# Kernel optimization log

Measured on AMD Instinct MI355X. Metric: run time of the kernel, lower is better.

Reference implementation:

```python
import jax, jax.numpy as jnp
import numpy as np

N_NODES = 50000
N_EDGES = 1600000


def _seg_softmax(e, seg, n):
    # numerically-stable softmax over edges grouped by destination node
    m = jax.ops.segment_max(e, seg, num_segments=n)
    ex = jnp.exp(e - m[seg])
    s = jax.ops.segment_sum(ex, seg, num_segments=n)
    return ex / s[seg]


def setup_inputs() -> dict:
    key = jax.random.key(0)
    ks = jax.random.split(key, 16)
    IN, OUT, ED = 64, 32, 8
    inp = {
        'x': jax.random.normal(ks[0], (N_NODES, IN), jnp.float32),
        'ex': jax.random.normal(ks[1], (N_EDGES, ED), jnp.float32),
        'src': jax.random.randint(ks[2], (N_EDGES,), 0, N_NODES),
        'dst': jax.random.randint(ks[3], (N_EDGES,), 0, N_NODES),
        'W_fc': jax.random.normal(ks[4], (OUT, IN), jnp.float32) * 0.1,
        'b_fc': jax.random.normal(ks[5], (OUT,), jnp.float32) * 0.1,
        'W_att': jax.random.normal(ks[6], (1, 2 * OUT + ED), jnp.float32) * 0.1,
        'b_att': jax.random.normal(ks[7], (1,), jnp.float32) * 0.1,
        'W_edge': jax.random.normal(ks[8], (OUT, ED), jnp.float32) * 0.1,
        'b_edge': jax.random.normal(ks[9], (OUT,), jnp.float32) * 0.1,
        'W_eatt': jax.random.normal(ks[10], (ED, ED), jnp.float32) * 0.1,
        'b_eatt': jax.random.normal(ks[11], (ED,), jnp.float32) * 0.1,
        'W_q': jax.random.normal(ks[12], (OUT, OUT), jnp.float32) * 0.1,
        'b_q': jax.random.normal(ks[13], (OUT,), jnp.float32) * 0.1,
        'W_s': jax.random.normal(ks[14], (OUT, OUT), jnp.float32) * 0.1,
        'b_s': jax.random.normal(ks[15], (OUT,), jnp.float32) * 0.1,
    }
    return inp


def reference(x, ex, src, dst, W_fc, b_fc, W_att, b_att, W_edge, b_edge,
              W_eatt, b_eatt, W_q, b_q, W_s, b_s):
    n = x.shape[0]
    # node transform (fc; batch norm disabled in config)
    z = x @ W_fc.T + b_fc                      # [N, OUT]
    z_src = z[src]                             # [E, OUT]
    z_dst = z[dst]                             # [E, OUT]
    # edge transform for attention score
    ex_t = ex @ W_eatt.T + b_eatt              # [E, ED]
    # edge-dependent attention logit + leaky_relu(0.2)
    z2 = jnp.concatenate([z_src, z_dst, ex_t], axis=1)  # [E, 2*OUT+ED]
    a = z2 @ W_att.T + b_att                   # [E, 1]
    e = jnp.where(a >= 0, a, 0.2 * a)
    # edge feature aggregation transform
    ez = ex @ W_edge.T + b_edge                # [E, OUT]
    # similar_node branch: pointwise conv1d == linear; per-edge dot product
    q = z_src @ W_q.T + b_q                    # query(src)
    s = z_dst @ W_s.T + b_s                    # support(dst)
    es = jnp.sum(q * s, axis=1, keepdims=True)  # [E, 1]
    # edge-softmax over incoming edges of each destination node
    alpha = _seg_softmax(e, dst, n)            # [E, 1]
    similar = _seg_softmax(es, dst, n)         # [E, 1]
    h_att = jax.ops.segment_sum(alpha * z_src, dst, num_segments=n)    # [N, OUT]
    h2 = jax.ops.segment_sum(similar * z_src, dst, num_segments=n)     # [N, OUT]
    h = h_att * h2
    # attention-weighted edge feature aggregation
    h = h + jax.ops.segment_sum(alpha * ez, dst, num_segments=n)
    return h, alpha
```

## Files before the change

kernel.cpp:

```cpp
#include <hip/hip_runtime.h>
#include <hip/hip_fp16.h>

#define OUTF 32
#define INF 64
#define EDF 8
#define CAP 64
#define BSH 7
#define NBKMAX 512
#define EPB 4096

__global__ __launch_bounds__(256) void prep_kernel(
    const float* __restrict__ x,
    const float* __restrict__ W_fc, const float* __restrict__ b_fc,
    const float* __restrict__ W_q,  const float* __restrict__ b_q,
    const float* __restrict__ W_s,  const float* __restrict__ b_s,
    const float* __restrict__ W_att,
    __half* __restrict__ z16, float* __restrict__ t,
    float* __restrict__ c_es,
    float* __restrict__ att_s, float* __restrict__ att_d,
    int* __restrict__ cursor, int* __restrict__ bhist, int n_nodes)
{
    int i = blockIdx.x * 256 + threadIdx.x;
    if (i < NBKMAX) bhist[i] = 0;
    if (i >= n_nodes) return;
    cursor[i] = i * CAP;
    int n = i;

    float xl[INF];
    for (int k = 0; k < INF; k++) xl[k] = x[(size_t)n * INF + k];

    float zl[OUTF];
    float a1 = 0.f, a2 = 0.f;
    for (int o = 0; o < OUTF; o++) {
        float acc = b_fc[o];
        for (int k = 0; k < INF; k++) acc += xl[k] * W_fc[o * INF + k];
        zl[o] = acc;
        z16[(size_t)n * OUTF + o] = __float2half(acc);
        a1 += acc * W_att[o];
        a2 += acc * W_att[OUTF + o];
    }
    att_s[n] = a1;
    att_d[n] = a2;

    float sl[OUTF];
    float ces = 0.f;
    for (int o = 0; o < OUTF; o++) {
        float as = b_s[o];
        for (int k = 0; k < OUTF; k++) as += zl[k] * W_s[o * OUTF + k];
        sl[o] = as;
        ces += b_q[o] * as;
    }
    c_es[n] = ces;
    for (int k = 0; k < OUTF; k++) {
        float tv = 0.f;
        for (int o = 0; o < OUTF; o++) tv += W_q[o * OUTF + k] * sl[o];
        t[(size_t)n * OUTF + k] = tv;
    }
}

__global__ __launch_bounds__(256) void bhist_kernel(
    const int* __restrict__ didx, int* __restrict__ bhist, int eBase, int eEnd)
{
    __shared__ int cnt[NBKMAX];
    for (int i = threadIdx.x; i < NBKMAX; i += 256) cnt[i] = 0;
    __syncthreads();
    int e0 = eBase + blockIdx.x * EPB;
    #pragma unroll 16
    for (int k = 0; k < 16; k++) {
        int e = e0 + k * 256 + threadIdx.x;
        if (e < eEnd) atomicAdd(&cnt[didx[e] >> BSH], 1);
    }
    __syncthreads();
    for (int i = threadIdx.x; i < NBKMAX; i += 256)
        if (cnt[i]) atomicAdd(&bhist[i], cnt[i]);
}

__global__ __launch_bounds__(512) void bscan_kernel(
    int* __restrict__ bhist, int* __restrict__ bbase,
    int* __restrict__ bcursor, int nbk)
{
    __shared__ int sh[512];
    int t = threadIdx.x;
    int v = (t < nbk) ? bhist[t] : 0;
    sh[t] = v;
    __syncthreads();
    for (int st = 1; st < 512; st <<= 1) {
        int tv = (t >= st) ? sh[t - st] : 0;
        __syncthreads();
        sh[t] += tv;
        __syncthreads();
    }
    if (t < nbk) {
        int excl = sh[t] - v;
        bbase[t] = excl;
        bcursor[t] = excl;
        bhist[t] = 0;
        if (t == nbk - 1) bbase[nbk] = sh[t];
    }
}

__global__ __launch_bounds__(256) void bin_kernel(
    const int* __restrict__ sidx, const int* __restrict__ didx,
    int* __restrict__ bcursor, int2* __restrict__ stage, int eBase, int eEnd)
{
    __shared__ int cnt[NBKMAX];
    __shared__ int gbase[NBKMAX];
    for (int i = threadIdx.x; i < NBKMAX; i += 256) cnt[i] = 0;
    __syncthreads();
    int e0 = eBase + blockIdx.x * EPB;
    int srcv[16], dstv[16], rankv[16];
    #pragma unroll 16
    for (int k = 0; k < 16; k++) {
        int e = e0 + k * 256 + threadIdx.x;
        if (e < eEnd) {
            srcv[k] = sidx[e]; dstv[k] = didx[e];
            rankv[k] = atomicAdd(&cnt[dstv[k] >> BSH], 1);
        } else srcv[k] = -1;
    }
    __syncthreads();
    for (int b = threadIdx.x; b < NBKMAX; b += 256)
        if (cnt[b]) gbase[b] = atomicAdd(&bcursor[b], cnt[b]);
    __syncthreads();
    #pragma unroll 16
    for (int k = 0; k < 16; k++) {
        if (srcv[k] >= 0) {
            int e = e0 + k * 256 + threadIdx.x;
            int b = dstv[k] >> BSH;
            stage[gbase[b] + rankv[k]] =
                make_int2(srcv[k], e | ((dstv[k] & 127) << 21));
        }
    }
}

__global__ __launch_bounds__(256) void place_kernel(
    const int* __restrict__ bbase, const int2* __restrict__ stage,
    int2* __restrict__ csr, int* __restrict__ cursor, int N)
{
    __shared__ int c[1 << BSH];
    int b = blockIdx.x;
    int nodeBase = b << BSH;
    int nNodes = min(1 << BSH, N - nodeBase);
    for (int i = threadIdx.x; i < nNodes; i += 256) c[i] = cursor[nodeBase + i];
    __syncthreads();
    int beg = bbase[b], end = bbase[b + 1];
    for (int j = beg + threadIdx.x; j < end; j += 256) {
        int2 r = stage[j];
        int dl  = (r.y >> 21) & 127;
        int eid = r.y & 0x1FFFFF;
        int pos = atomicAdd(&c[dl], 1);
        if (pos < (nodeBase + dl) * CAP + CAP)
            csr[pos] = make_int2(r.x, eid);
    }
    __syncthreads();
    for (int i = threadIdx.x; i < nNodes; i += 256) {
        int lim = (nodeBase + i) * CAP + CAP;
        cursor[nodeBase + i] = min(c[i], lim);
    }
}

__device__ __forceinline__ float4 loadHalf4(const __half* p) {
    uint2 raw = *(const uint2*)p;
    __half2 h01 = *reinterpret_cast<__half2*>(&raw.x);
    __half2 h23 = *reinterpret_cast<__half2*>(&raw.y);
    float2 f01 = __half22float2(h01);
    float2 f23 = __half22float2(h23);
    return make_float4(f01.x, f01.y, f23.x, f23.y);
}

__global__ __launch_bounds__(256) void agg_kernel(
    const int* __restrict__ cursor, const int2* __restrict__ csr,
    const float* __restrict__ att_d, const float* __restrict__ c_es,
    const __half* __restrict__ z16, const float* __restrict__ t,
    const float* __restrict__ ex,
    const float* __restrict__ W_att, const float* __restrict__ b_att,
    const float* __restrict__ W_eatt, const float* __restrict__ b_eatt,
    const float* __restrict__ W_edge, const float* __restrict__ b_edge,
    float* __restrict__ h_out, float* __restrict__ invS_out, int N)
{
    __shared__ float sv3[EDF];
    __shared__ float ccs;
    __shared__ float sWedge[OUTF * EDF];
    __shared__ float sbedge[OUTF];
    int tid = threadIdx.x;
    if (tid < EDF) {
        float a = 0.f;
        for (int j = 0; j < EDF; j++) a += W_att[2 * OUTF + j] * W_eatt[j * EDF + tid];
        sv3[tid] = a;
    }
    if (tid == 0) {
        float a = b_att[0];
        for (int j = 0; j < EDF; j++) a += W_att[2 * OUTF + j] * b_eatt[j];
        ccs = a;
    }
    if (tid < OUTF * EDF) sWedge[tid] = W_edge[tid];
    if (tid < OUTF) sbedge[tid] = b_edge[tid];
    __syncthreads();

    int wave = blockIdx.x * 4 + (tid >> 6);
    if (wave >= N) return;
    int lane = tid & 63;
    int g = lane >> 3;
    int l = lane & 7;
    int n = wave;
    int beg = n * CAP, end = cursor[n];

    float4 t4  = *(const float4*)(t + (size_t)n * OUTF + l * 4);
    float4 wa4 = *(const float4*)(W_att + l * 4);
    float4 v34 = (l < 2) ? *(const float4*)(sv3 + l * 4)
                         : make_float4(0.f, 0.f, 0.f, 0.f);
    float attc = att_d[n] + ccs;
    float cesn = c_es[n];

    float S = 0.f, Spe = 0.f;
    float4 U1 = make_float4(0.f, 0.f, 0.f, 0.f);
    float4 U2 = U1, Uax = U1;

    for (int p0 = beg; p0 < end; p0 += 16) {
        int posA = p0 + g;
        bool vA = posA < end;
        int2 ceA = csr[vA ? posA : beg];
        int posB = p0 + 8 + g;
        bool vB = posB < end;
        int2 ceB = csr[vB ? posB : beg];

        float4 zA = loadHalf4(z16 + (size_t)ceA.x * OUTF + l * 4);
        float4 zB = loadHalf4(z16 + (size_t)ceB.x * OUTF + l * 4);
        float4 eA = (l < 2) ? *(const float4*)(ex + (size_t)ceA.y * EDF + l * 4)
                            : make_float4(0.f, 0.f, 0.f, 0.f);
        float4 eB = (l < 2) ? *(const float4*)(ex + (size_t)ceB.y * EDF + l * 4)
                            : make_float4(0.f, 0.f, 0.f, 0.f);

        float rA = zA.x * t4.x + zA.y * t4.y + zA.z * t4.z + zA.w * t4.w;
        float mA = zA.x * wa4.x + zA.y * wa4.y + zA.z * wa4.z + zA.w * wa4.w
                 + eA.x * v34.x + eA.y * v34.y + eA.z * v34.z + eA.w * v34.w;
        float rB = zB.x * t4.x + zB.y * t4.y + zB.z * t4.z + zB.w * t4.w;
        float mB = zB.x * wa4.x + zB.y * wa4.y + zB.z * wa4.z + zB.w * wa4.w
                 + eB.x * v34.x + eB.y * v34.y + eB.z * v34.z + eB.w * v34.w;
        #pragma unroll
        for (int m = 4; m >= 1; m >>= 1) {
            rA += __shfl_xor(rA, m);
            mA += __shfl_xor(mA, m);
            rB += __shfl_xor(rB, m);
            mB += __shfl_xor(mB, m);
        }
        float aA = mA + attc;
        float aB = mB + attc;
        float pA  = vA ? __expf(aA >= 0.f ? aA : 0.2f * aA) : 0.f;
        float peA = vA ? __expf(rA + cesn) : 0.f;
        float pB  = vB ? __expf(aB >= 0.f ? aB : 0.2f * aB) : 0.f;
        float peB = vB ? __expf(rB + cesn) : 0.f;

        S += pA + pB; Spe += peA + peB;
        U1.x += pA * zA.x + pB * zB.x;  U1.y += pA * zA.y + pB * zB.y;
        U1.z += pA * zA.z + pB * zB.z;  U1.w += pA * zA.w + pB * zB.w;
        U2.x += peA * zA.x + peB * zB.x; U2.y += peA * zA.y + peB * zB.y;
        U2.z += peA * zA.z + peB * zB.z; U2.w += peA * zA.w + peB * zB.w;
        Uax.x += pA * eA.x + pB * eB.x; Uax.y += pA * eA.y + pB * eB.y;
        Uax.z += pA * eA.z + pB * eB.z; Uax.w += pA * eA.w + pB * eB.w;
    }

    #pragma unroll
    for (int m = 8; m <= 32; m <<= 1) {
        S   += __shfl_xor(S, m);
        Spe += __shfl_xor(Spe, m);
        U1.x += __shfl_xor(U1.x, m); U1.y += __shfl_xor(U1.y, m);
        U1.z += __shfl_xor(U1.z, m); U1.w += __shfl_xor(U1.w, m);
        U2.x += __shfl_xor(U2.x, m); U2.y += __shfl_xor(U2.y, m);
        U2.z += __shfl_xor(U2.z, m); U2.w += __shfl_xor(U2.w, m);
        Uax.x += __shfl_xor(Uax.x, m); Uax.y += __shfl_xor(Uax.y, m);
        Uax.z += __shfl_xor(Uax.z, m); Uax.w += __shfl_xor(Uax.w, m);
    }

    float invS = 0.f;
    float4 h4 = make_float4(0.f, 0.f, 0.f, 0.f);
    if (end > beg) {
        invS = 1.f / S;
        float invSpe = 1.f / Spe;
        float ax[EDF];
        ax[0] = __shfl(Uax.x, 0); ax[1] = __shfl(Uax.y, 0);
        ax[2] = __shfl(Uax.z, 0); ax[3] = __shfl(Uax.w, 0);
        ax[4] = __shfl(Uax.x, 1); ax[5] = __shfl(Uax.y, 1);
        ax[6] = __shfl(Uax.z, 1); ax[7] = __shfl(Uax.w, 1);
        #pragma unroll
        for (int j = 0; j < 4; j++) {
            int c = l * 4 + j;
            float hagg = sbedge[c];
            #pragma unroll
            for (int k = 0; k < EDF; k++)
                hagg += sWedge[c * EDF + k] * (ax[k] * invS);
            float hatt = ((j == 0) ? U1.x : (j == 1) ? U1.y : (j == 2) ? U1.z : U1.w) * invS;
            float h2   = ((j == 0) ? U2.x : (j == 1) ? U2.y : (j == 2) ? U2.z : U2.w) * invSpe;
            ((float*)&h4)[j] = hatt * h2 + hagg;
        }
    }
    if (lane < 8) {
        *(float4*)(h_out + (size_t)n * OUTF + l * 4) = h4;
        if (lane == 0) invS_out[n] = invS;
    }
}

__global__ __launch_bounds__(256) void alpha_kernel(
    const int* __restrict__ sidx, const int* __restrict__ didx,
    const float* __restrict__ ex,
    const float* __restrict__ att_s, const float* __restrict__ att_d,
    const float* __restrict__ invS,
    const float* __restrict__ W_att, const float* __restrict__ b_att,
    const float* __restrict__ W_eatt, const float* __restrict__ b_eatt,
    float* __restrict__ alpha_out, int E)
{
    __shared__ float v3[EDF];
    __shared__ float ccs;
    int tid = threadIdx.x;
    if (tid < EDF) {
        float a = 0.f;
        for (int j = 0; j < EDF; j++) a += W_att[2 * OUTF + j] * W_eatt[j * EDF + tid];
        v3[tid] = a;
    }
    if (tid == 0) {
        float a = b_att[0];
        for (int j = 0; j < EDF; j++) a += W_att[2 * OUTF + j] * b_eatt[j];
        ccs = a;
    }
    __syncthreads();

    int e = blockIdx.x * 256 + tid;
    if (e >= E) return;
    int si = sidx[e], di = didx[e];
    const float4* exr = (const float4*)(ex + (size_t)e * EDF);
    float4 e0 = exr[0], e1 = exr[1];
    float a = att_s[si] + att_d[di] + ccs
            + e0.x * v3[0] + e0.y * v3[1] + e0.z * v3[2] + e0.w * v3[3]
            + e1.x * v3[4] + e1.y * v3[5] + e1.z * v3[6] + e1.w * v3[7];
    float el = (a >= 0.f) ? a : 0.2f * a;
    alpha_out[e] = __expf(el) * invS[di];
}

extern "C" void kernel_launch(void* const* d_in, const int* in_sizes, int n_in,
                              void* d_out, int out_size, void* d_ws, size_t ws_size,
                              hipStream_t stream) {
    const float* x      = (const float*)d_in[0];
    const float* ex     = (const float*)d_in[1];
    const int*   sidx   = (const int*)d_in[2];
    const int*   didx   = (const int*)d_in[3];
    const float* W_fc   = (const float*)d_in[4];
    const float* b_fc   = (const float*)d_in[5];
    const float* W_att  = (const float*)d_in[6];
    const float* b_att  = (const float*)d_in[7];
    const float* W_edge = (const float*)d_in[8];
    const float* b_edge = (const float*)d_in[9];
    const float* W_eatt = (const float*)d_in[10];
    const float* b_eatt = (const float*)d_in[11];
    const float* W_q    = (const float*)d_in[12];
    const float* b_q    = (const float*)d_in[13];
    const float* W_s    = (const float*)d_in[14];
    const float* b_s    = (const float*)d_in[15];

    int N = in_sizes[0] / INF;
    int E = in_sizes[2];
    int N32 = N * OUTF;
    int nbk = (N + (1 << BSH) - 1) >> BSH;

    float* h_out     = (float*)d_out;
    float* alpha_out = h_out + N32;

    float*  base    = (float*)d_ws;
    int*    cursor  = (int*)base;
    float*  att_s   = base + N;
    float*  att_d   = att_s + N;
    float*  invS    = att_d + N;
    float*  c_es    = invS + N;
    __half* z16     = (__half*)(c_es + N);
    float*  t       = (float*)(z16 + (size_t)N * OUTF);

    size_t fixedBytes = (size_t)N * (20 + 64 + 128 + CAP * 8) + 8192;
    int halfE = (E + 1) / 2;
    int stageElems = (ws_size >= fixedBytes + (size_t)E * 8) ? E : halfE;
    int phases = (stageElems == E) ? 1 : 2;

    int2*  stage   = (int2*)(t + N32);
    int2*  csr     = stage + stageElems;
    int*   bhist   = (int*)(csr + (size_t)N * CAP);
    int*   bbase   = bhist + NBKMAX;
    int*   bcursor = bbase + NBKMAX + 1;

    prep_kernel<<<(N + 255) / 256, 256, 0, stream>>>(
        x, W_fc, b_fc, W_q, b_q, W_s, b_s, W_att,
        z16, t, c_es, att_s, att_d, cursor, bhist, N);

    for (int ph = 0; ph < phases; ph++) {
        int eB = ph * stageElems;
        int eE = (eB + stageElems < E) ? eB + stageElems : E;
        int nbC = (eE - eB + EPB - 1) / EPB;
        bhist_kernel<<<nbC, 256, 0, stream>>>(didx, bhist, eB, eE);
        bscan_kernel<<<1, 512, 0, stream>>>(bhist, bbase, bcursor, nbk);
        bin_kernel<<<nbC, 256, 0, stream>>>(sidx, didx, bcursor, stage, eB, eE);
        place_kernel<<<nbk, 256, 0, stream>>>(bbase, stage, csr, cursor, N);
    }

    int nbAgg = (N + 3) / 4;
    agg_kernel<<<nbAgg, 256, 0, stream>>>(
        cursor, csr, att_d, c_es,
        z16, t, ex,
        W_att, b_att, W_eatt, b_eatt, W_edge, b_edge,
        h_out, invS, N);

    int nbE = (E + 255) / 256;
    alpha_kernel<<<nbE, 256, 0, stream>>>(
        sidx, didx, ex, att_s, att_d, invS,
        W_att, b_att, W_eatt, b_eatt, alpha_out, E);
}
```

Baseline: 188.1 us.

## Replace fixed-capacity CSR with compact per-node CSR and fp16 staged edge features

Drops the fixed CAP=64 slots per node and instead computes exact per-node offsets with a per-bucket count and scan in place_kernel, producing a compact index list. Edge features are gathered during binning and stored as fp16 in bucket order, so the aggregation reads them from nearly contiguous staging memory instead of doing random fp32 reads of ex. Bucket size is halved to 64 nodes and the two-phase workspace fallback is removed. The risks are that the workspace must now hold all staged data at once, fp16 edge features lose precision, and packing src into 16 bits only works for node ids below 65536.

```diff
diff --git a/kernel.cpp b/kernel.cpp
--- a/kernel.cpp
+++ b/kernel.cpp
@@ -4,9 +4,9 @@
 #define OUTF 32
 #define INF 64
 #define EDF 8
-#define CAP 64
-#define BSH 7
-#define NBKMAX 512
+#define BSH 6
+#define BN  (1 << BSH)
+#define NBKMAX 1024
 #define EPB 4096
 
 __global__ __launch_bounds__(256) void prep_kernel(
@@ -18,12 +18,11 @@
     __half* __restrict__ z16, float* __restrict__ t,
     float* __restrict__ c_es,
     float* __restrict__ att_s, float* __restrict__ att_d,
-    int* __restrict__ cursor, int* __restrict__ bhist, int n_nodes)
+    int* __restrict__ bhist, int n_nodes)
 {
     int i = blockIdx.x * 256 + threadIdx.x;
     if (i < NBKMAX) bhist[i] = 0;
     if (i >= n_nodes) return;
-    cursor[i] = i * CAP;
     int n = i;
 
     float xl[INF];
@@ -59,32 +58,32 @@
 }
 
 __global__ __launch_bounds__(256) void bhist_kernel(
-    const int* __restrict__ didx, int* __restrict__ bhist, int eBase, int eEnd)
+    const int* __restrict__ didx, int* __restrict__ bhist, int E)
 {
     __shared__ int cnt[NBKMAX];
     for (int i = threadIdx.x; i < NBKMAX; i += 256) cnt[i] = 0;
     __syncthreads();
-    int e0 = eBase + blockIdx.x * EPB;
+    int e0 = blockIdx.x * EPB;
     #pragma unroll 16
     for (int k = 0; k < 16; k++) {
         int e = e0 + k * 256 + threadIdx.x;
-        if (e < eEnd) atomicAdd(&cnt[didx[e] >> BSH], 1);
+        if (e < E) atomicAdd(&cnt[didx[e] >> BSH], 1);
     }
     __syncthreads();
     for (int i = threadIdx.x; i < NBKMAX; i += 256)
         if (cnt[i]) atomicAdd(&bhist[i], cnt[i]);
 }
 
-__global__ __launch_bounds__(512) void bscan_kernel(
-    int* __restrict__ bhist, int* __restrict__ bbase,
+__global__ __launch_bounds__(1024) void bscan_kernel(
+    const int* __restrict__ bhist, int* __restrict__ bbase,
     int* __restrict__ bcursor, int nbk)
 {
-    __shared__ int sh[512];
+    __shared__ int sh[1024];
     int t = threadIdx.x;
     int v = (t < nbk) ? bhist[t] : 0;
     sh[t] = v;
     __syncthreads();
-    for (int st = 1; st < 512; st <<= 1) {
+    for (int st = 1; st < 1024; st <<= 1) {
         int tv = (t >= st) ? sh[t - st] : 0;
         __syncthreads();
         sh[t] += tv;
@@ -94,25 +93,31 @@
         int excl = sh[t] - v;
         bbase[t] = excl;
         bcursor[t] = excl;
-        bhist[t] = 0;
         if (t == nbk - 1) bbase[nbk] = sh[t];
     }
+}
+
+__device__ __forceinline__ unsigned pack2h(float a, float b) {
+    __half2 h = __floats2half2_rn(a, b);
+    return *(unsigned*)&h;
 }
 
 __global__ __launch_bounds__(256) void bin_kernel(
     const int* __restrict__ sidx, const int* __restrict__ didx,
-    int* __restrict__ bcursor, int2* __restrict__ stage, int eBase, int eEnd)
+    const float* __restrict__ ex,
+    int* __restrict__ bcursor, int* __restrict__ stage_meta,
+    uint4* __restrict__ stage_ex, int E)
 {
     __shared__ int cnt[NBKMAX];
     __shared__ int gbase[NBKMAX];
     for (int i = threadIdx.x; i < NBKMAX; i += 256) cnt[i] = 0;
     __syncthreads();
-    int e0 = eBase + blockIdx.x * EPB;
+    int e0 = blockIdx.x * EPB;
     int srcv[16], dstv[16], rankv[16];
     #pragma unroll 16
     for (int k = 0; k < 16; k++) {
         int e = e0 + k * 256 + threadIdx.x;
-        if (e < eEnd) {
+        if (e < E) {
             srcv[k] = sidx[e]; dstv[k] = didx[e];
             rankv[k] = atomicAdd(&cnt[dstv[k] >> BSH], 1);
         } else srcv[k] = -1;
@@ -126,35 +131,57 @@
         if (srcv[k] >= 0) {
             int e = e0 + k * 256 + threadIdx.x;
             int b = dstv[k] >> BSH;
-            stage[gbase[b] + rankv[k]] =
-                make_int2(srcv[k], e | ((dstv[k] & 127) << 21));
+            int pos = gbase[b] + rankv[k];
+            stage_meta[pos] = srcv[k] | ((dstv[k] & (BN - 1)) << 16);
+            const float4* exr = (const float4*)(ex + (size_t)e * EDF);
+            float4 a = exr[0], c = exr[1];
+            stage_ex[pos] = make_uint4(pack2h(a.x, a.y), pack2h(a.z, a.w),
+                                       pack2h(c.x, c.y), pack2h(c.z, c.w));
         }
     }
 }
 
 __global__ __launch_bounds__(256) void place_kernel(
-    const int* __restrict__ bbase, const int2* __restrict__ stage,
-    int2* __restrict__ csr, int* __restrict__ cursor, int N)
-{
-    __shared__ int c[1 << BSH];
+    const int* __restrict__ bbase, const int* __restrict__ stage_meta,
+    int* __restrict__ csr_pos, int* __restrict__ nodeStart,
+    int* __restrict__ nodeCnt, int N)
+{
+    __shared__ int cnt[BN], excl[BN], cur[BN], scan[BN];
+    int tid = threadIdx.x;
     int b = blockIdx.x;
     int nodeBase = b << BSH;
-    int nNodes = min(1 << BSH, N - nodeBase);
-    for (int i = threadIdx.x; i < nNodes; i += 256) c[i] = cursor[nodeBase + i];
-    __syncthreads();
     int beg = bbase[b], end = bbase[b + 1];
-    for (int j = beg + threadIdx.x; j < end; j += 256) {
-        int2 r = stage[j];
-        int dl  = (r.y >> 21) & 127;
-        int eid = r.y & 0x1FFFFF;
-        int pos = atomicAdd(&c[dl], 1);
-        if (pos < (nodeBase + dl) * CAP + CAP)
-            csr[pos] = make_int2(r.x, eid);
-    }
-    __syncthreads();
-    for (int i = threadIdx.x; i < nNodes; i += 256) {
-        int lim = (nodeBase + i) * CAP + CAP;
-        cursor[nodeBase + i] = min(c[i], lim);
+
+    if (tid < BN) cnt[tid] = 0;
+    __syncthreads();
+    for (int j = beg + tid; j < end; j += 256)
+        atomicAdd(&cnt[(stage_meta[j] >> 16) & (BN - 1)], 1);
+    __syncthreads();
+    if (tid < BN) scan[tid] = cnt[tid];
+    __syncthreads();
+    for (int st = 1; st < BN; st <<= 1) {
+        int v = (tid < BN && tid >= st) ? scan[tid - st] : 0;
+        __syncthreads();
+        if (tid < BN) scan[tid] += v;
+        __syncthreads();
+    }
+    if (tid < BN) {
+        excl[tid] = scan[tid] - cnt[tid];
+        cur[tid] = excl[tid];
+    }
+    __syncthreads();
+    for (int j = beg + tid; j < end; j += 256) {
+        int dl = (stage_meta[j] >> 16) & (BN - 1);
+        int pos = atomicAdd(&cur[dl], 1);
+        csr_pos[beg + pos] = j;
+    }
+    __syncthreads();
+    if (tid < BN) {
+        int n = nodeBase + tid;
+        if (n < N) {
+            nodeStart[n] = beg + excl[tid];
+            nodeCnt[n] = cnt[tid];
+        }
     }
 }
 
@@ -166,12 +193,17 @@
     float2 f23 = __half22float2(h23);
     return make_float4(f01.x, f01.y, f23.x, f23.y);
 }
+__device__ __forceinline__ float2 unp2(unsigned u) {
+    __half2 h = *reinterpret_cast<__half2*>(&u);
+    return __half22float2(h);
+}
 
 __global__ __launch_bounds__(256) void agg_kernel(
-    const int* __restrict__ cursor, const int2* __restrict__ csr,
+    const int* __restrict__ nodeStart, const int* __restrict__ nodeCnt,
+    const int* __restrict__ csr_pos,
+    const int* __restrict__ stage_meta, const uint4* __restrict__ stage_ex,
     const float* __restrict__ att_d, const float* __restrict__ c_es,
     const __half* __restrict__ z16, const float* __restrict__ t,
-    const float* __restrict__ ex,
     const float* __restrict__ W_att, const float* __restrict__ b_att,
     const float* __restrict__ W_eatt, const float* __restrict__ b_eatt,
     const float* __restrict__ W_edge, const float* __restrict__ b_edge,
@@ -202,7 +234,7 @@
     int g = lane >> 3;
     int l = lane & 7;
     int n = wave;
-    int beg = n * CAP, end = cursor[n];
+    int beg = nodeStart[n], ec = nodeCnt[n];
 
     float4 t4  = *(const float4*)(t + (size_t)n * OUTF + l * 4);
     float4 wa4 = *(const float4*)(W_att + l * 4);
@@ -215,20 +247,27 @@
     float4 U1 = make_float4(0.f, 0.f, 0.f, 0.f);
     float4 U2 = U1, Uax = U1;
 
-    for (int p0 = beg; p0 < end; p0 += 16) {
-        int posA = p0 + g;
-        bool vA = posA < end;
-        int2 ceA = csr[vA ? posA : beg];
-        int posB = p0 + 8 + g;
-        bool vB = posB < end;
-        int2 ceB = csr[vB ? posB : beg];
-
-        float4 zA = loadHalf4(z16 + (size_t)ceA.x * OUTF + l * 4);
-        float4 zB = loadHalf4(z16 + (size_t)ceB.x * OUTF + l * 4);
-        float4 eA = (l < 2) ? *(const float4*)(ex + (size_t)ceA.y * EDF + l * 4)
-                            : make_float4(0.f, 0.f, 0.f, 0.f);
-        float4 eB = (l < 2) ? *(const float4*)(ex + (size_t)ceB.y * EDF + l * 4)
-                            : make_float4(0.f, 0.f, 0.f, 0.f);
+    for (int e0 = 0; e0 < ec; e0 += 16) {
+        int jA = e0 + g;
+        bool vA = jA < ec;
+        int idxA = csr_pos[beg + (vA ? jA : 0)];
+        int jB = e0 + 8 + g;
+        bool vB = jB < ec;
+        int idxB = csr_pos[beg + (vB ? jB : 0)];
+
+        int srcA = stage_meta[idxA] & 0xFFFF;
+        int srcB = stage_meta[idxB] & 0xFFFF;
+        uint4 ejA = stage_ex[idxA];
+        uint4 ejB = stage_ex[idxB];
+
+        float4 zA = loadHalf4(z16 + (size_t)srcA * OUTF + l * 4);
+        float4 zB = loadHalf4(z16 + (size_t)srcB * OUTF + l * 4);
+        float4 eA, eB;
+        if (l == 0) { float2 p0 = unp2(ejA.x), p1 = unp2(ejA.y); eA = make_float4(p0.x, p0.y, p1.x, p1.y);
+                      float2 q0 = unp2(ejB.x), q1 = unp2(ejB.y); eB = make_float4(q0.x, q0.y, q1.x, q1.y); }
+        else if (l == 1) { float2 p0 = unp2(ejA.z), p1 = unp2(ejA.w); eA = make_float4(p0.x, p0.y, p1.x, p1.y);
+                           float2 q0 = unp2(ejB.z), q1 = unp2(ejB.w); eB = make_float4(q0.x, q0.y, q1.x, q1.y); }
+        else { eA = make_float4(0.f, 0.f, 0.f, 0.f); eB = eA; }
 
         float rA = zA.x * t4.x + zA.y * t4.y + zA.z * t4.z + zA.w * t4.w;
         float mA = zA.x * wa4.x + zA.y * wa4.y + zA.z * wa4.z + zA.w * wa4.w
@@ -273,7 +312,7 @@
 
     float invS = 0.f;
     float4 h4 = make_float4(0.f, 0.f, 0.f, 0.f);
-    if (end > beg) {
+    if (ec > 0) {
         invS = 1.f / S;
         float invSpe = 1.f / Spe;
         float ax[EDF];
@@ -358,49 +397,43 @@
     int N = in_sizes[0] / INF;
     int E = in_sizes[2];
     int N32 = N * OUTF;
-    int nbk = (N + (1 << BSH) - 1) >> BSH;
+    int nbk = (N + BN - 1) >> BSH;
 
     float* h_out     = (float*)d_out;
     float* alpha_out = h_out + N32;
 
     float*  base    = (float*)d_ws;
-    int*    cursor  = (int*)base;
-    float*  att_s   = base + N;
+    float*  att_s   = base;
     float*  att_d   = att_s + N;
     float*  invS    = att_d + N;
     float*  c_es    = invS + N;
     __half* z16     = (__half*)(c_es + N);
     float*  t       = (float*)(z16 + (size_t)N * OUTF);
-
-    size_t fixedBytes = (size_t)N * (20 + 64 + 128 + CAP * 8) + 8192;
-    int halfE = (E + 1) / 2;
-    int stageElems = (ws_size >= fixedBytes + (size_t)E * 8) ? E : halfE;
-    int phases = (stageElems == E) ? 1 : 2;
-
-    int2*  stage   = (int2*)(t + N32);
-    int2*  csr     = stage + stageElems;
-    int*   bhist   = (int*)(csr + (size_t)N * CAP);
-    int*   bbase   = bhist + NBKMAX;
-    int*   bcursor = bbase + NBKMAX + 1;
+    int*    nodeStart = (int*)(t + N32);
+    int*    nodeCnt   = nodeStart + N;
+    int*    stage_meta = nodeCnt + N;
+    uint4*  stage_ex   = (uint4*)(stage_meta + E);
+    int*    csr_pos = (int*)(stage_ex + E);
+    int*    bhist   = csr_pos + E;
+    int*    bbase   = bhist + NBKMAX;
+    int*    bcursor = bbase + NBKMAX + 1;
 
     prep_kernel<<<(N + 255) / 256, 256, 0, stream>>>(
         x, W_fc, b_fc, W_q, b_q, W_s, b_s, W_att,
-        z16, t, c_es, att_s, att_d, cursor, bhist, N);
-
-    for (int ph = 0; ph < phases; ph++) {
-        int eB = ph * stageElems;
-        int eE = (eB + stageElems < E) ? eB + stageElems : E;
-        int nbC = (eE - eB + EPB - 1) / EPB;
-        bhist_kernel<<<nbC, 256, 0, stream>>>(didx, bhist, eB, eE);
-        bscan_kernel<<<1, 512, 0, stream>>>(bhist, bbase, bcursor, nbk);
-        bin_kernel<<<nbC, 256, 0, stream>>>(sidx, didx, bcursor, stage, eB, eE);
-        place_kernel<<<nbk, 256, 0, stream>>>(bbase, stage, csr, cursor, N);
-    }
+        z16, t, c_es, att_s, att_d, bhist, N);
+
+    int nbC = (E + EPB - 1) / EPB;
+    bhist_kernel<<<nbC, 256, 0, stream>>>(didx, bhist, E);
+    bscan_kernel<<<1, 1024, 0, stream>>>(bhist, bbase, bcursor, nbk);
+    bin_kernel<<<nbC, 256, 0, stream>>>(sidx, didx, ex, bcursor,
+                                        stage_meta, stage_ex, E);
+    place_kernel<<<nbk, 256, 0, stream>>>(bbase, stage_meta, csr_pos,
+                                          nodeStart, nodeCnt, N);
 
     int nbAgg = (N + 3) / 4;
     agg_kernel<<<nbAgg, 256, 0, stream>>>(
-        cursor, csr, att_d, c_es,
-        z16, t, ex,
+        nodeStart, nodeCnt, csr_pos, stage_meta, stage_ex,
+        att_d, c_es, z16, t,
         W_att, b_att, W_eatt, b_eatt, W_edge, b_edge,
         h_out, invS, N);
 
```

After: 222.3 us. +18.2%, slower.
